# Optimization experiments

Hardware: AMD Instinct MI355X
Metric: run time of the kernel (lower is better)

## Reference

```python
import jax, jax.numpy as jnp
import numpy as np

N, D, C = 1_000_000, 128, 1000


def setup_inputs() -> dict:
    key = jax.random.key(0)
    k1, k2, k3 = jax.random.split(key, 3)
    x = jax.random.normal(k1, (N, D), dtype=jnp.float32)
    anchors = jax.random.normal(k2, (C, D), dtype=jnp.float32)
    y = jax.random.randint(k3, (N,), 0, C, dtype=jnp.int64)
    return {"x": x, "anchors": anchors, "y": y}


def reference(x, anchors, y):
    # Per-sample squared distance to the anchor of its label: ||x_i - a_{y_i}||^2
    diff = x - anchors[y]                      # [N, D] gather + subtract
    d = jnp.sum(diff * diff, axis=1)           # [N]
    # Torch loop: per present label l, loss_l = mean_i(||x_i - a_l||^2 / c_l)
    #           = (1/c_l^2) * sum_{i: y_i=l} ||x_i - a_l||^2 ; total = sum_l loss_l
    seg_sum = jax.ops.segment_sum(d, y, num_segments=C)                      # [C]
    counts = jax.ops.segment_sum(jnp.ones_like(d), y, num_segments=C)        # [C]
    per_class = jnp.where(counts > 0, seg_sum / (counts * counts), 0.0)
    return jnp.sum(per_class)
```

## Files before the change

### kernel.cpp

```cpp
#include <hip/hip_runtime.h>

#define DDIM 128

__global__ __launch_bounds__(256) void dist_kernel(
    const float* __restrict__ x, const float* __restrict__ anchors,
    const int* __restrict__ y,
    float* __restrict__ pseg, unsigned* __restrict__ pcnt,
    int n, int C)
{
    extern __shared__ char smem[];
    float*    segL = (float*)smem;
    unsigned* cntL = (unsigned*)(smem + (size_t)C * sizeof(float));

    for (int c = threadIdx.x; c < C; c += blockDim.x) { segL[c] = 0.0f; cntL[c] = 0u; }
    __syncthreads();

    const int tid  = blockIdx.x * blockDim.x + threadIdx.x;
    const int wave = tid >> 6;
    const int lane = threadIdx.x & 63;
    const int g    = lane >> 4;
    const int q    = lane & 15;
    const int totalWaves = (gridDim.x * blockDim.x) >> 6;
    const int stride = totalWaves * 8;

    for (int base = wave * 8; base < n; base += stride) {
        const int i0 = base + g;
        const int i1 = i0 + 4;
        const bool v0 = i0 < n, v1 = i1 < n;

        int l0 = 0, l1 = 0;
        if (v0) l0 = y[i0];
        if (v1) l1 = y[i1];

        float4 xa0, xa1, xb0, xb1;
        float4 aa0, aa1, ab0, ab1;
        if (v0) {
            const float4* xp = (const float4*)(x + (size_t)i0 * DDIM + q * 8);
            xa0 = xp[0]; xa1 = xp[1];
        }
        if (v1) {
            const float4* xp = (const float4*)(x + (size_t)i1 * DDIM + q * 8);
            xb0 = xp[0]; xb1 = xp[1];
        }
        if (v0) {
            const float4* ap = (const float4*)(anchors + (size_t)l0 * DDIM + q * 8);
            aa0 = ap[0]; aa1 = ap[1];
        }
        if (v1) {
            const float4* ap = (const float4*)(anchors + (size_t)l1 * DDIM + q * 8);
            ab0 = ap[0]; ab1 = ap[1];
        }

        float acc0 = 0.0f, acc1 = 0.0f;
        if (v0) {
            float d;
            d = xa0.x - aa0.x; acc0 = fmaf(d, d, acc0);
            d = xa0.y - aa0.y; acc0 = fmaf(d, d, acc0);
            d = xa0.z - aa0.z; acc0 = fmaf(d, d, acc0);
            d = xa0.w - aa0.w; acc0 = fmaf(d, d, acc0);
            d = xa1.x - aa1.x; acc0 = fmaf(d, d, acc0);
            d = xa1.y - aa1.y; acc0 = fmaf(d, d, acc0);
            d = xa1.z - aa1.z; acc0 = fmaf(d, d, acc0);
            d = xa1.w - aa1.w; acc0 = fmaf(d, d, acc0);
        }
        if (v1) {
            float d;
            d = xb0.x - ab0.x; acc1 = fmaf(d, d, acc1);
            d = xb0.y - ab0.y; acc1 = fmaf(d, d, acc1);
            d = xb0.z - ab0.z; acc1 = fmaf(d, d, acc1);
            d = xb0.w - ab0.w; acc1 = fmaf(d, d, acc1);
            d = xb1.x - ab1.x; acc1 = fmaf(d, d, acc1);
            d = xb1.y - ab1.y; acc1 = fmaf(d, d, acc1);
            d = xb1.z - ab1.z; acc1 = fmaf(d, d, acc1);
            d = xb1.w - ab1.w; acc1 = fmaf(d, d, acc1);
        }

        #pragma unroll
        for (int off = 1; off < 16; off <<= 1) {
            acc0 += __shfl_xor(acc0, off);
            acc1 += __shfl_xor(acc1, off);
        }
        if (q == 0) {
            if (v0) { atomicAdd(&segL[l0], acc0); atomicAdd(&cntL[l0], 1u); }
            if (v1) { atomicAdd(&segL[l1], acc1); atomicAdd(&cntL[l1], 1u); }
        }
    }
    __syncthreads();

    float*    myseg = pseg + (size_t)blockIdx.x * C;
    unsigned* mycnt = pcnt + (size_t)blockIdx.x * C;
    for (int c = threadIdx.x; c < C; c += blockDim.x) {
        myseg[c] = segL[c];
        mycnt[c] = cntL[c];
    }
}

__global__ __launch_bounds__(256) void reduceB4_kernel(
    const float4* __restrict__ pseg4, const uint4* __restrict__ pcnt4,
    float4* __restrict__ sseg4, float4* __restrict__ scnt4,
    int B, int C4, int rowsPerSlice)
{
    const int c4 = blockIdx.x * 256 + threadIdx.x;
    if (c4 >= C4) return;
    const int slice = blockIdx.y;
    const int b0 = slice * rowsPerSlice;
    int b1 = b0 + rowsPerSlice; if (b1 > B) b1 = B;

    float4 s = {0.f, 0.f, 0.f, 0.f};
    float4 k = {0.f, 0.f, 0.f, 0.f};
    for (int b = b0; b < b1; ++b) {
        float4 ps = pseg4[(size_t)b * C4 + c4];
        uint4  pc = pcnt4[(size_t)b * C4 + c4];
        s.x += ps.x; s.y += ps.y; s.z += ps.z; s.w += ps.w;
        k.x += (float)pc.x; k.y += (float)pc.y; k.z += (float)pc.z; k.w += (float)pc.w;
    }
    sseg4[(size_t)slice * C4 + c4] = s;
    scnt4[(size_t)slice * C4 + c4] = k;
}

__global__ __launch_bounds__(256) void reduceB_kernel(
    const float* __restrict__ pseg, const unsigned* __restrict__ pcnt,
    float* __restrict__ sseg, float* __restrict__ scnt,
    int B, int C, int rowsPerSlice)
{
    const int c = blockIdx.x * 256 + threadIdx.x;
    if (c >= C) return;
    const int slice = blockIdx.y;
    const int b0 = slice * rowsPerSlice;
    int b1 = b0 + rowsPerSlice; if (b1 > B) b1 = B;

    float s = 0.0f, k = 0.0f;
    for (int b = b0; b < b1; ++b) {
        s += pseg[(size_t)b * C + c];
        k += (float)pcnt[(size_t)b * C + c];
    }
    sseg[(size_t)slice * C + c] = s;
    scnt[(size_t)slice * C + c] = k;
}

__global__ __launch_bounds__(1024) void finalize_kernel(
    const float* __restrict__ sseg, const float* __restrict__ scnt,
    float* __restrict__ out, int nslice, int C)
{
    __shared__ float red[1024];
    const int t = threadIdx.x;
    float v = 0.0f;
    for (int c = t; c < C; c += 1024) {
        float s = 0.0f, k = 0.0f;
        for (int sl = 0; sl < nslice; ++sl) {
            s += sseg[(size_t)sl * C + c];
            k += scnt[(size_t)sl * C + c];
        }
        if (k > 0.0f) v += s / (k * k);
    }
    red[t] = v;
    __syncthreads();
    #pragma unroll
    for (int st = 512; st > 0; st >>= 1) {
        if (t < st) red[t] += red[t + st];
        __syncthreads();
    }
    if (t == 0) out[0] = red[0];
}

extern "C" void kernel_launch(void* const* d_in, const int* in_sizes, int n_in,
                              void* d_out, int out_size, void* d_ws, size_t ws_size,
                              hipStream_t stream) {
    const float* x       = (const float*)d_in[0];
    const float* anchors = (const float*)d_in[1];
    const int*   y       = (const int*)d_in[2];
    float*       out     = (float*)d_out;

    const int n = in_sizes[2];
    const int C = in_sizes[1] / DDIM;

    const int rowsPerSlice = 64;

    long long cap = ((long long)ws_size) / ((long long)C * 8 + (long long)C * 16 / rowsPerSlice + 16);
    int B = (int)(cap < 1 ? 1 : (cap > 1024 ? 1024 : cap));
    const int nslice = (B + rowsPerSlice - 1) / rowsPerSlice;

    float*    pseg = (float*)d_ws;
    unsigned* pcnt = (unsigned*)((char*)d_ws + (size_t)B * C * 4);
    float*    sseg = (float*)((char*)d_ws + (size_t)B * C * 8);
    float*    scnt = (float*)((char*)d_ws + (size_t)B * C * 8 + (size_t)nslice * C * 4);

    const size_t ldsBytes = (size_t)C * 8;
    dist_kernel<<<B, 256, ldsBytes, stream>>>(x, anchors, y, pseg, pcnt, n, C);

    if ((C & 3) == 0) {
        const int C4 = C >> 2;
        dim3 gridB((C4 + 255) / 256, nslice);
        reduceB4_kernel<<<gridB, 256, 0, stream>>>(
            (const float4*)pseg, (const uint4*)pcnt,
            (float4*)sseg, (float4*)scnt, B, C4, rowsPerSlice);
    } else {
        dim3 gridB((C + 255) / 256, nslice);
        reduceB_kernel<<<gridB, 256, 0, stream>>>(pseg, pcnt, sseg, scnt, B, C, rowsPerSlice);
    }

    finalize_kernel<<<1, 1024, 0, stream>>>(sseg, scnt, out, nslice, C);
}
```

Measured before the change: 144.9 us.

## Map 32 lanes per row with one float4 each and double grid blocks

The distance kernel now assigns 32 lanes per row, each loading one float4, so a wave covers 4 rows per iteration instead of 8 rows with two float4 loads per lane. Bounds checks are removed from the main loop and handled in a separate tail block. The block cap rises from 1024 to 2048 to add parallelism. The trade-off is less memory-level parallelism per thread, more shuffle steps per row, and twice as many partial rows for the reduction kernels to sum.

```diff
diff --git a/kernel.cpp b/kernel.cpp
--- a/kernel.cpp
+++ b/kernel.cpp
@@ -18,71 +18,81 @@
     const int tid  = blockIdx.x * blockDim.x + threadIdx.x;
     const int wave = tid >> 6;
     const int lane = threadIdx.x & 63;
-    const int g    = lane >> 4;
-    const int q    = lane & 15;
+    const int half = lane >> 5;
+    const int c4   = lane & 31;
     const int totalWaves = (gridDim.x * blockDim.x) >> 6;
-    const int stride = totalWaves * 8;
-
-    for (int base = wave * 8; base < n; base += stride) {
-        const int i0 = base + g;
-        const int i1 = i0 + 4;
-        const bool v0 = i0 < n, v1 = i1 < n;
-
-        int l0 = 0, l1 = 0;
-        if (v0) l0 = y[i0];
-        if (v1) l1 = y[i1];
-
-        float4 xa0, xa1, xb0, xb1;
-        float4 aa0, aa1, ab0, ab1;
-        if (v0) {
-            const float4* xp = (const float4*)(x + (size_t)i0 * DDIM + q * 8);
-            xa0 = xp[0]; xa1 = xp[1];
-        }
-        if (v1) {
-            const float4* xp = (const float4*)(x + (size_t)i1 * DDIM + q * 8);
-            xb0 = xp[0]; xb1 = xp[1];
-        }
-        if (v0) {
-            const float4* ap = (const float4*)(anchors + (size_t)l0 * DDIM + q * 8);
-            aa0 = ap[0]; aa1 = ap[1];
-        }
-        if (v1) {
-            const float4* ap = (const float4*)(anchors + (size_t)l1 * DDIM + q * 8);
-            ab0 = ap[0]; ab1 = ap[1];
-        }
-
-        float acc0 = 0.0f, acc1 = 0.0f;
-        if (v0) {
-            float d;
-            d = xa0.x - aa0.x; acc0 = fmaf(d, d, acc0);
-            d = xa0.y - aa0.y; acc0 = fmaf(d, d, acc0);
-            d = xa0.z - aa0.z; acc0 = fmaf(d, d, acc0);
-            d = xa0.w - aa0.w; acc0 = fmaf(d, d, acc0);
-            d = xa1.x - aa1.x; acc0 = fmaf(d, d, acc0);
-            d = xa1.y - aa1.y; acc0 = fmaf(d, d, acc0);
-            d = xa1.z - aa1.z; acc0 = fmaf(d, d, acc0);
-            d = xa1.w - aa1.w; acc0 = fmaf(d, d, acc0);
-        }
-        if (v1) {
-            float d;
-            d = xb0.x - ab0.x; acc1 = fmaf(d, d, acc1);
-            d = xb0.y - ab0.y; acc1 = fmaf(d, d, acc1);
-            d = xb0.z - ab0.z; acc1 = fmaf(d, d, acc1);
-            d = xb0.w - ab0.w; acc1 = fmaf(d, d, acc1);
-            d = xb1.x - ab1.x; acc1 = fmaf(d, d, acc1);
-            d = xb1.y - ab1.y; acc1 = fmaf(d, d, acc1);
-            d = xb1.z - ab1.z; acc1 = fmaf(d, d, acc1);
-            d = xb1.w - ab1.w; acc1 = fmaf(d, d, acc1);
-        }
+    const int rowStride = totalWaves * 4;
+
+    const float4* x4 = (const float4*)x;
+    const float4* a4 = (const float4*)anchors;
+
+    int R = wave * 4;
+    for (; R + 4 <= n; R += rowStride) {
+        const int rA = R + half;
+        const int rB = rA + 2;
+
+        const int lA = y[rA];
+        const int lB = y[rB];
+
+        float4 xa = x4[rA * 32 + c4];
+        float4 xb = x4[rB * 32 + c4];
+        float4 aa = a4[lA * 32 + c4];
+        float4 ab = a4[lB * 32 + c4];
+
+        float acc0 = 0.0f, acc1 = 0.0f, d;
+        d = xa.x - aa.x; acc0 = fmaf(d, d, acc0);
+        d = xa.y - aa.y; acc0 = fmaf(d, d, acc0);
+        d = xa.z - aa.z; acc0 = fmaf(d, d, acc0);
+        d = xa.w - aa.w; acc0 = fmaf(d, d, acc0);
+        d = xb.x - ab.x; acc1 = fmaf(d, d, acc1);
+        d = xb.y - ab.y; acc1 = fmaf(d, d, acc1);
+        d = xb.z - ab.z; acc1 = fmaf(d, d, acc1);
+        d = xb.w - ab.w; acc1 = fmaf(d, d, acc1);
 
         #pragma unroll
-        for (int off = 1; off < 16; off <<= 1) {
+        for (int off = 1; off < 32; off <<= 1) {
             acc0 += __shfl_xor(acc0, off);
             acc1 += __shfl_xor(acc1, off);
         }
-        if (q == 0) {
-            if (v0) { atomicAdd(&segL[l0], acc0); atomicAdd(&cntL[l0], 1u); }
-            if (v1) { atomicAdd(&segL[l1], acc1); atomicAdd(&cntL[l1], 1u); }
+        if (c4 == 0) {
+            atomicAdd(&segL[lA], acc0); atomicAdd(&cntL[lA], 1u);
+            atomicAdd(&segL[lB], acc1); atomicAdd(&cntL[lB], 1u);
+        }
+    }
+
+    if (R < n) {
+        const int rA = R + half;
+        const int rB = rA + 2;
+        const bool vA = rA < n, vB = rB < n;
+        int lA = 0, lB = 0;
+        if (vA) lA = y[rA];
+        if (vB) lB = y[rB];
+
+        float acc0 = 0.0f, acc1 = 0.0f, d;
+        if (vA) {
+            float4 xa = x4[rA * 32 + c4];
+            float4 aa = a4[lA * 32 + c4];
+            d = xa.x - aa.x; acc0 = fmaf(d, d, acc0);
+            d = xa.y - aa.y; acc0 = fmaf(d, d, acc0);
+            d = xa.z - aa.z; acc0 = fmaf(d, d, acc0);
+            d = xa.w - aa.w; acc0 = fmaf(d, d, acc0);
+        }
+        if (vB) {
+            float4 xb = x4[rB * 32 + c4];
+            float4 ab = a4[lB * 32 + c4];
+            d = xb.x - ab.x; acc1 = fmaf(d, d, acc1);
+            d = xb.y - ab.y; acc1 = fmaf(d, d, acc1);
+            d = xb.z - ab.z; acc1 = fmaf(d, d, acc1);
+            d = xb.w - ab.w; acc1 = fmaf(d, d, acc1);
+        }
+        #pragma unroll
+        for (int off = 1; off < 32; off <<= 1) {
+            acc0 += __shfl_xor(acc0, off);
+            acc1 += __shfl_xor(acc1, off);
+        }
+        if (c4 == 0) {
+            if (vA) { atomicAdd(&segL[lA], acc0); atomicAdd(&cntL[lA], 1u); }
+            if (vB) { atomicAdd(&segL[lB], acc1); atomicAdd(&cntL[lB], 1u); }
         }
     }
     __syncthreads();
@@ -177,7 +187,7 @@
     const int rowsPerSlice = 64;
 
     long long cap = ((long long)ws_size) / ((long long)C * 8 + (long long)C * 16 / rowsPerSlice + 16);
-    int B = (int)(cap < 1 ? 1 : (cap > 1024 ? 1024 : cap));
+    int B = (int)(cap < 1 ? 1 : (cap > 2048 ? 2048 : cap));
     const int nslice = (B + rowsPerSlice - 1) / rowsPerSlice;
 
     float*    pseg = (float*)d_ws;
```

New measurement: 136.1 us. 1.06x faster.
